# Performance work log

Measured on AMD Instinct MI355X. Metric: run time of the kernel, lower is better.

Reference implementation:

```python
import jax, jax.numpy as jnp
import numpy as np

NUM_HEADS = 8

def setup_inputs() -> dict:
    key = jax.random.key(0)
    ks = jax.random.split(key, 8)
    B, T, J, N, C = 4, 16, 17, 17, 256
    x = jax.random.normal(ks[0], (B, T, J, N, C), dtype=jnp.float32)
    A_s = jax.random.uniform(ks[1], (J, J), dtype=jnp.float32)
    A_v = jax.random.uniform(ks[2], (N, N), dtype=jnp.float32)
    W_qkv = jax.random.normal(ks[3], (C, 5 * C), dtype=jnp.float32) * (C ** -0.5)
    W_proj = jax.random.normal(ks[4], (3 * C, C), dtype=jnp.float32) * ((3 * C) ** -0.5)
    b_proj = jnp.zeros((C,), dtype=jnp.float32)
    # M ~ xavier_uniform(gain=1.414) over shape (1, J, N, C)
    bound = 1.414 * np.sqrt(6.0 / (N + C))
    M = jax.random.uniform(ks[5], (1, J, N, C), dtype=jnp.float32, minval=-bound, maxval=bound)
    adj_s = jnp.full((J, J), 1e-6, dtype=jnp.float32)  # torch stores (1,1,J,J); broadcast-identical
    adj_v = jnp.full((N, N), 1e-6, dtype=jnp.float32)
    return {"x": x, "A_s": A_s, "A_v": A_v, "W_qkv": W_qkv, "W_proj": W_proj,
            "b_proj": b_proj, "M": M, "adj_s": adj_s, "adj_v": adj_v}


def reference(x, A_s, A_v, W_qkv, W_proj, b_proj, M, adj_s, adj_v):
    B, T, J, N, C = x.shape
    h = NUM_HEADS
    hc = C // h
    scale = hc ** -0.5
    bt = B * T
    xr = x.reshape(bt, J, N, C)
    # qkv Linear (no bias) then view(..., C, 5): channel-interleaved split
    qkv = (xr @ W_qkv).reshape(bt, J, N, C, 5)
    q, k, vs, vv, vsv = (qkv[..., i] * M for i in range(5))
    def heads(t):
        return t.reshape(bt, J, N, h, hc)
    q, k, vs, vv, vsv = map(heads, (q, k, vs, vv, vsv))
    # spatial attention over joints j (per node n), temporal/variate attention over n (per j)
    att_s_o = jnp.einsum('bjnhc,bknhc->bhnjk', q, k) * scale   # (bt,h,N,J,J)
    att_v_o = jnp.einsum('bjnhc,bjmhc->bhjnm', q, k) * scale   # (bt,h,J,N,N)
    att_s = jax.nn.softmax(att_s_o, axis=-1)
    att_v = jax.nn.softmax(att_v_o, axis=-1)
    # outer-product combine, algebraically separated:
    # x_vsv[b,j,n,:] = sum_{k,m} att_s[b,h,n,j,k] * att_v[b,h,j,n,m] * vsv[b,k,m,h,:]
    r = jnp.einsum('bhjnm,bkmhc->bhjnkc', att_v, vsv)           # (bt,h,J,N,J,hc)
    x_vsv = jnp.einsum('bhnjk,bhjnkc->bjnhc', att_s, r).reshape(bt, J, N, C)
    # adjacency-biased attentions (symmetrized learned bias + fixed adjacency)
    adjs = A_s + adj_s
    adjs = (adjs.T + adjs) * 0.5
    adjv = A_v + adj_v
    adjv = (adjv.T + adjv) * 0.5
    att_s2 = jax.nn.softmax(att_s_o + adjs, axis=-1)
    att_v2 = jax.nn.softmax(att_v_o + adjv, axis=-1)
    x_vs = jnp.einsum('bhnjk,bknhc->bjnhc', att_s2, vs).reshape(bt, J, N, C)
    x_vv = jnp.einsum('bhjnm,bjmhc->bjnhc', att_v2, vv).reshape(bt, J, N, C)
    out = jnp.concatenate([x_vsv, x_vs, x_vv], axis=-1) @ W_proj + b_proj
    return out.reshape(B, T, J, N, C)
```

## Files before the change

### kernel.cpp

```cpp
#include <hip/hip_runtime.h>
#include <math.h>

#define ROWS 18496
#define SCALE 0.17677669529663687f

typedef unsigned short ushort_t;
typedef __attribute__((ext_vector_type(8))) short short8;
typedef __attribute__((ext_vector_type(4))) float f32x4;

__device__ __forceinline__ void fma4(float4& d, float s, const float4& v) {
    d.x = fmaf(s, v.x, d.x); d.y = fmaf(s, v.y, d.y);
    d.z = fmaf(s, v.z, d.z); d.w = fmaf(s, v.w, d.w);
}
__device__ __forceinline__ float dot4(const float4& a, const float4& b) {
    return a.x*b.x + a.y*b.y + a.z*b.z + a.w*b.w;
}

__device__ __forceinline__ ushort_t f2bf(float x) {
    union { float f; unsigned u; } v; v.f = x;
    unsigned r = v.u + 0x7fffu + ((v.u >> 16) & 1u);
    return (ushort_t)(r >> 16);
}
__device__ __forceinline__ float bf2f(ushort_t b) {
    union { unsigned u; float f; } v; v.u = ((unsigned)b) << 16; return v.f;
}

__device__ __forceinline__ unsigned cvtpk(float a, float b) {
    unsigned r;
    asm("v_cvt_pk_bf16_f32 %0, %1, %2" : "=v"(r) : "v"(a), "v"(b));
    return r;
}
__device__ __forceinline__ float uasf(unsigned u) {
    union { unsigned u; float f; } v; v.u = u; return v.f;
}

__device__ __forceinline__ void gl_lds16(const void* g, void* l) {
    __builtin_amdgcn_global_load_lds(
        (const __attribute__((address_space(1))) void*)g,
        (__attribute__((address_space(3))) void*)l, 16, 0, 0);
}

__device__ __forceinline__ void store_hilo(ushort_t* yhi, ushort_t* ylo,
                                           size_t off, const float4& a)
{
    unsigned h01 = cvtpk(a.x, a.y), h23 = cvtpk(a.z, a.w);
    unsigned l01 = cvtpk(a.x - uasf(h01 << 16), a.y - uasf(h01 & 0xffff0000u));
    unsigned l23 = cvtpk(a.z - uasf(h23 << 16), a.w - uasf(h23 & 0xffff0000u));
    *(uint2*)&yhi[off] = (uint2){h01, h23};
    *(uint2*)&ylo[off] = (uint2){l01, l23};
}

__global__ __launch_bounds__(256) void k_cvt_w(
    const float* __restrict__ W, ushort_t* __restrict__ bh, ushort_t* __restrict__ bl,
    const float* __restrict__ Wp, ushort_t* __restrict__ wph, ushort_t* __restrict__ wpl)
{
    if (blockIdx.x < 1280) {
        int o = blockIdx.x;
        int kk = threadIdx.x;
        int col = (o & 255) * 5 + (o >> 8);
        float v = W[(size_t)kk * 1280 + col];
        ushort_t hh = f2bf(v);
        bh[(size_t)o * 256 + kk] = hh;
        bl[(size_t)o * 256 + kk] = f2bf(v - bf2f(hh));
    } else {
        int n = blockIdx.x - 1280;
        for (int k = threadIdx.x; k < 768; k += 256) {
            float v = Wp[(size_t)k * 256 + n];
            ushort_t h = f2bf(v);
            wph[(size_t)n * 768 + k] = h;
            wpl[(size_t)n * 768 + k] = f2bf(v - bf2f(h));
        }
    }
}

template<int BM, int BN, int K, int MODE>
__global__ __launch_bounds__(256) void k_gemm(
    const float* __restrict__ Af,
    const ushort_t* __restrict__ Ahi, const ushort_t* __restrict__ Alo,
    const ushort_t* __restrict__ Bhi, const ushort_t* __restrict__ Blo,
    const float* __restrict__ aux,
    float* __restrict__ out)
{
    constexpr int MT = BM / 32;
    constexpr int NT = BN / 32;
    __shared__ __attribute__((aligned(16))) ushort_t sAh[BM * 32];
    __shared__ __attribute__((aligned(16))) ushort_t sAl[BM * 32];
    __shared__ __attribute__((aligned(16))) ushort_t sBh[BN * 32];
    __shared__ __attribute__((aligned(16))) ushort_t sBl[BN * 32];

    const int t = threadIdx.x;
    const int lane = t & 63;
    const int ln = lane & 15, quad = lane >> 4;
    const int wave = t >> 6;
    const int wm = wave >> 1, wn = wave & 1;

    const int nwg = (int)(gridDim.x * gridDim.y);
    int wgid = (int)(blockIdx.y * gridDim.x + blockIdx.x);
    int q = nwg >> 3, r = nwg & 7;
    int xcd = wgid & 7, i0 = wgid >> 3;
    int base = (xcd < r) ? xcd * (q + 1) : r * (q + 1) + (xcd - r) * q;
    int logical = base + i0;
    const int m0 = (logical / (int)gridDim.x) * BM;
    const int n0 = (logical % (int)gridDim.x) * BN;

    f32x4 acc[MT][NT];
#pragma unroll
    for (int i = 0; i < MT; ++i)
#pragma unroll
        for (int j = 0; j < NT; ++j) acc[i][j] = (f32x4){0.f, 0.f, 0.f, 0.f};

    float4 a0r, a1r, a2r, a3r;
    size_t a_base = 0;
    if (MODE == 0) {
        int row = t >> 1, kc8 = t & 1;
        int gr = m0 + row; if (gr > ROWS - 1) gr = ROWS - 1;
        a_base = (size_t)gr * K + kc8 * 16;
        const float* src = &Af[a_base];
        a0r = *(const float4*)&src[0];
        a1r = *(const float4*)&src[4];
        a2r = *(const float4*)&src[8];
        a3r = *(const float4*)&src[12];
    }

    for (int kb = 0; kb < K; kb += 32) {
        __syncthreads();
        if (MODE == 0) {
            unsigned h0 = cvtpk(a0r.x, a0r.y), h1 = cvtpk(a0r.z, a0r.w);
            unsigned h2 = cvtpk(a1r.x, a1r.y), h3 = cvtpk(a1r.z, a1r.w);
            unsigned h4 = cvtpk(a2r.x, a2r.y), h5 = cvtpk(a2r.z, a2r.w);
            unsigned h6 = cvtpk(a3r.x, a3r.y), h7 = cvtpk(a3r.z, a3r.w);
            unsigned l0 = cvtpk(a0r.x - uasf(h0 << 16), a0r.y - uasf(h0 & 0xffff0000u));
            unsigned l1 = cvtpk(a0r.z - uasf(h1 << 16), a0r.w - uasf(h1 & 0xffff0000u));
            unsigned l2 = cvtpk(a1r.x - uasf(h2 << 16), a1r.y - uasf(h2 & 0xffff0000u));
            unsigned l3 = cvtpk(a1r.z - uasf(h3 << 16), a1r.w - uasf(h3 & 0xffff0000u));
            unsigned l4 = cvtpk(a2r.x - uasf(h4 << 16), a2r.y - uasf(h4 & 0xffff0000u));
            unsigned l5 = cvtpk(a2r.z - uasf(h5 << 16), a2r.w - uasf(h5 & 0xffff0000u));
            unsigned l6 = cvtpk(a3r.x - uasf(h6 << 16), a3r.y - uasf(h6 & 0xffff0000u));
            unsigned l7 = cvtpk(a3r.z - uasf(h7 << 16), a3r.w - uasf(h7 & 0xffff0000u));
            uint4* dh = (uint4*)((char*)sAh + (size_t)t * 32);
            uint4* dl = (uint4*)((char*)sAl + (size_t)t * 32);
            dh[0] = (uint4){h0, h1, h2, h3};
            dh[1] = (uint4){h4, h5, h6, h7};
            dl[0] = (uint4){l0, l1, l2, l3};
            dl[1] = (uint4){l4, l5, l6, l7};
        } else {
#pragma unroll
            for (int s = t; s < BM * 4; s += 256) {
                int row = s >> 2, kc = s & 3;
                int gr = m0 + row; if (gr > ROWS - 1) gr = ROWS - 1;
                size_t gb = ((size_t)gr * K + kb) * 2 + kc * 16;
                int lb = (s & ~63) * 16;
                gl_lds16((const char*)Ahi + gb, (char*)sAh + lb);
                gl_lds16((const char*)Alo + gb, (char*)sAl + lb);
            }
        }
#pragma unroll
        for (int s = t; s < BN * 4; s += 256) {
            int row = s >> 2, kc = s & 3;
            size_t gb = ((size_t)(n0 + row) * K + kb) * 2 + kc * 16;
            int lb = (s & ~63) * 16;
            gl_lds16((const char*)Bhi + gb, (char*)sBh + lb);
            gl_lds16((const char*)Blo + gb, (char*)sBl + lb);
        }
        __syncthreads();

        if (MODE == 0 && kb + 32 < K) {
            const float* src = &Af[a_base + kb + 32];
            a0r = *(const float4*)&src[0];
            a1r = *(const float4*)&src[4];
            a2r = *(const float4*)&src[8];
            a3r = *(const float4*)&src[12];
        }

        short8 ah[MT], al[MT], bh[NT], bl[NT];
#pragma unroll
        for (int i = 0; i < MT; ++i) {
            int off = (wm * (BM / 2) + i * 16 + ln) * 32 + quad * 8;
            ah[i] = *(const short8*)&sAh[off];
            al[i] = *(const short8*)&sAl[off];
        }
#pragma unroll
        for (int j = 0; j < NT; ++j) {
            int off = (wn * (BN / 2) + j * 16 + ln) * 32 + quad * 8;
            bh[j] = *(const short8*)&sBh[off];
            bl[j] = *(const short8*)&sBl[off];
        }
#pragma unroll
        for (int i = 0; i < MT; ++i)
#pragma unroll
            for (int j = 0; j < NT; ++j) {
                acc[i][j] = __builtin_amdgcn_mfma_f32_16x16x32_bf16(ah[i], bh[j], acc[i][j], 0, 0, 0);
                acc[i][j] = __builtin_amdgcn_mfma_f32_16x16x32_bf16(ah[i], bl[j], acc[i][j], 0, 0, 0);
                acc[i][j] = __builtin_amdgcn_mfma_f32_16x16x32_bf16(al[i], bh[j], acc[i][j], 0, 0, 0);
            }
    }

#pragma unroll
    for (int i = 0; i < MT; ++i) {
#pragma unroll
        for (int r2 = 0; r2 < 4; ++r2) {
            int gm = m0 + wm * (BM / 2) + i * 16 + quad * 4 + r2;
            if (gm >= ROWS) continue;
            if (MODE == 0) {
                int jn = gm % 289;
                const float* Mrow = &aux[(size_t)jn * 256];
#pragma unroll
                for (int j = 0; j < NT; ++j) {
                    int gn = n0 + wn * (BN / 2) + j * 16 + ln;
                    out[(size_t)gm * 1280 + gn] = acc[i][j][r2] * Mrow[gn & 255];
                }
            } else {
#pragma unroll
                for (int j = 0; j < NT; ++j) {
                    int gn = n0 + wn * (BN / 2) + j * 16 + ln;
                    out[(size_t)gm * 256 + gn] = acc[i][j][r2] + aux[gn];
                }
            }
        }
    }
}

__global__ __launch_bounds__(512, 4) void k_att(
    const float* __restrict__ qkv5,
    const float* __restrict__ A_s, const float* __restrict__ A_v,
    const float* __restrict__ adjS, const float* __restrict__ adjV,
    ushort_t* __restrict__ yhi, ushort_t* __restrict__ ylo)
{
    __shared__ __attribute__((aligned(16))) float sm[17340];
    float* aS  = sm;
    float* aV  = sm + 4913;
    float* ebS = sm + 9826;
    float* ebV = sm + 10115;
    float* buf = sm + 10404;

    const int t  = threadIdx.x;
    const int bh = blockIdx.x;
    const int b  = bh >> 3, h = bh & 7;
    const size_t rowbase = (size_t)b * 289;

    for (int idx = t; idx < 578; idx += 512) {
        int f = idx / 289, rem = idx % 289;
        int jj = rem / 17, kk = rem % 17;
        float bias;
        if (f == 0)
            bias = 0.5f * ((A_s[jj*17+kk] + adjS[jj*17+kk]) + (A_s[kk*17+jj] + adjS[kk*17+jj]));
        else
            bias = 0.5f * ((A_v[jj*17+kk] + adjV[jj*17+kk]) + (A_v[kk*17+jj] + adjV[kk*17+jj]));
        (f ? ebV : ebS)[rem] = expf(bias);
    }

    for (int ch = 0; ch < 2; ++ch) {
        __syncthreads();
        for (int idx = t; idx < 1156; idx += 512) {
            int p = idx >> 2, c = idx & 3;
            *(float4*)&buf[p * 20 + c * 4] =
                *(const float4*)&qkv5[(rowbase + p) * 1280 + 256 + h * 32 + ch * 16 + c * 4];
        }
        __syncthreads();
        for (int u = t; u < 578; u += 512) {
            const bool isS = (u < 289);
            const int p = isS ? u : u - 289;
            const float* qp = &qkv5[(rowbase + p) * 1280 + h * 32 + ch * 16];
            float4 q0 = *(const float4*)&qp[0];
            float4 q1 = *(const float4*)&qp[4];
            float4 q2 = *(const float4*)&qp[8];
            float4 q3 = *(const float4*)&qp[12];
            const int a = p / 17, bb = p % 17;
            if (isS) {
                float* dst = &aS[bb * 289 + a * 17];
#pragma unroll
                for (int kk = 0; kk < 17; ++kk) {
                    const float4* r = (const float4*)&buf[(kk * 17 + bb) * 20];
                    float val = dot4(q0, r[0]) + dot4(q1, r[1]) + dot4(q2, r[2]) + dot4(q3, r[3]);
                    if (ch == 0) dst[kk] = val; else dst[kk] += val;
                }
            } else {
                float* dst = &aV[a * 289 + bb * 17];
#pragma unroll
                for (int mm = 0; mm < 17; ++mm) {
                    const float4* r = (const float4*)&buf[(a * 17 + mm) * 20];
                    float val = dot4(q0, r[0]) + dot4(q1, r[1]) + dot4(q2, r[2]) + dot4(q3, r[3]);
                    if (ch == 0) dst[mm] = val; else dst[mm] += val;
                }
            }
        }
    }
    __syncthreads();

    for (int idx = t; idx < 578; idx += 512) {
        float* row = (idx < 289) ? &aS[idx * 17] : &aV[(idx - 289) * 17];
        float mx = row[0];
#pragma unroll
        for (int kk = 1; kk < 17; ++kk) mx = fmaxf(mx, row[kk]);
        float sum = 0.f;
#pragma unroll
        for (int kk = 0; kk < 17; ++kk) {
            float e = expf((row[kk] - mx) * SCALE);
            row[kk] = e; sum += e;
        }
        float inv = 1.f / sum;
#pragma unroll
        for (int kk = 0; kk < 17; ++kk) row[kk] *= inv;
    }

    {
        const int lane = t & 63;
        const int ln = lane & 15, quad = lane >> 4;
        const int wave = t >> 6;
        ushort_t* vh = (ushort_t*)buf;
        ushort_t* vl = vh + 32 * 168;

        f32x4 acc[3][2];
#pragma unroll
        for (int r = 0; r < 3; ++r) {
            acc[r][0] = (f32x4){0.f,0.f,0.f,0.f};
            acc[r][1] = (f32x4){0.f,0.f,0.f,0.f};
        }

        int sbase[3], vbase[3];
#pragma unroll
        for (int r = 0; r < 3; ++r) {
            int p = (wave + 8 * r) * 16 + ln; if (p > 288) p = 288;
            int jj = (p * 61681) >> 20;
            int nn = p - jj * 17;
            sbase[r] = nn * 289 + jj * 17;
            vbase[r] = jj * 289 + nn * 17;
        }

        for (int khalf = 0; khalf < 2; ++khalf) {
            const int qbase = khalf * 160;
            const int V = khalf ? 129 : 160;
            __syncthreads();
            if (khalf == 1) {
                uint4* z = (uint4*)vh;
                for (int e = t; e < 1344; e += 512) z[e] = (uint4){0,0,0,0};
                __syncthreads();
            }
            for (int e = t; e < 32 * V; e += 512) {
                int ql = e >> 5, c = e & 31;
                float v = qkv5[(rowbase + qbase + ql) * 1280 + 1024 + h * 32 + c];
                unsigned hp = cvtpk(v, v);
                float lo = v - uasf(hp << 16);
                unsigned lp = cvtpk(lo, lo);
                vh[c * 168 + ql] = (ushort_t)hp;
                vl[c * 168 + ql] = (ushort_t)lp;
            }
            __syncthreads();
#pragma unroll
            for (int kstep = 0; kstep < 5; ++kstep) {
                const int q0 = qbase + kstep * 32 + quad * 8;
                const int lb = kstep * 32 + quad * 8;
#pragma unroll
                for (int r = 0; r < 3; ++r) {
                    if (r == 2 && wave >= 3) continue;
                    union { short8 s; unsigned u[4]; } A, L;
                    int qc0 = (q0 < 289) ? q0 : 288;
                    int k17 = (qc0 * 61681) >> 20;
                    int m17 = qc0 - k17 * 17;
                    float sv = aS[sbase[r] + k17];
#pragma unroll
                    for (int i2 = 0; i2 < 4; ++i2) {
                        float pv0 = sv * aV[vbase[r] + m17];
                        ++m17; if (m17 == 17) { m17 = 0; ++k17; sv = aS[sbase[r] + k17]; }
                        float pv1 = sv * aV[vbase[r] + m17];
                        ++m17; if (m17 == 17) { m17 = 0; ++k17; sv = aS[sbase[r] + k17]; }
                        if (khalf == 1) {
                            if (q0 + 2 * i2     >= 289) pv0 = 0.f;
                            if (q0 + 2 * i2 + 1 >= 289) pv1 = 0.f;
                        }
                        unsigned hp = cvtpk(pv0, pv1);
                        unsigned lp = cvtpk(pv0 - uasf(hp << 16),
                                            pv1 - uasf(hp & 0xffff0000u));
                        A.u[i2] = hp; L.u[i2] = lp;
                    }
#pragma unroll
                    for (int ct = 0; ct < 2; ++ct) {
                        short8 bh8 = *(const short8*)&vh[(ct * 16 + ln) * 168 + lb];
                        short8 bl8 = *(const short8*)&vl[(ct * 16 + ln) * 168 + lb];
                        acc[r][ct] = __builtin_amdgcn_mfma_f32_16x16x32_bf16(A.s, bh8, acc[r][ct], 0, 0, 0);
                        acc[r][ct] = __builtin_amdgcn_mfma_f32_16x16x32_bf16(A.s, bl8, acc[r][ct], 0, 0, 0);
                        acc[r][ct] = __builtin_amdgcn_mfma_f32_16x16x32_bf16(L.s, bh8, acc[r][ct], 0, 0, 0);
                    }
                }
            }
        }
#pragma unroll
        for (int r = 0; r < 3; ++r) {
            int rt = wave + 8 * r;
            if (rt >= 19) continue;
#pragma unroll
            for (int ct = 0; ct < 2; ++ct) {
#pragma unroll
                for (int rr = 0; rr < 4; ++rr) {
                    int p = rt * 16 + quad * 4 + rr;
                    if (p > 288) continue;
                    float v = acc[r][ct][rr];
                    unsigned hp = cvtpk(v, v);
                    float lo = v - uasf(hp << 16);
                    unsigned lp = cvtpk(lo, lo);
                    size_t off = (rowbase + p) * 768 + h * 32 + ct * 16 + ln;
                    yhi[off] = (ushort_t)hp;
                    ylo[off] = (ushort_t)lp;
                }
            }
        }
    }

    __syncthreads();
    for (int idx = t; idx < 578; idx += 512) {
        float* row;
        const float* eb;
        if (idx < 289) { row = &aS[idx * 17]; eb = &ebS[(idx % 17) * 17]; }
        else { int i2 = idx - 289; row = &aV[i2 * 17]; eb = &ebV[(i2 % 17) * 17]; }
        float s = 0.f;
#pragma unroll
        for (int kk = 0; kk < 17; ++kk) { float wv = row[kk] * eb[kk]; row[kk] = wv; s += wv; }
        float inv = 1.f / s;
#pragma unroll
        for (int kk = 0; kk < 17; ++kk) row[kk] *= inv;
    }

    for (int ch = 0; ch < 2; ++ch) {
        __syncthreads();
        for (int idx = t; idx < 1156; idx += 512) {
            int p = idx >> 2, c = idx & 3;
            *(float4*)&buf[p * 24 + c * 4] =
                *(const float4*)&qkv5[(rowbase + p) * 1280 + 512 + h * 32 + ch * 16 + c * 4];
        }
        __syncthreads();
        for (int u = t; u < 1156; u += 512) {
            const int c4 = (u & 3) * 4, rest = u >> 2;
            const int n = rest % 17, j = rest / 17;
            const float* as = &aS[n * 289 + j * 17];
            float4 a0 = {0,0,0,0};
            for (int kk = 0; kk < 17; ++kk) {
                float4 v = *(const float4*)&buf[(kk * 17 + n) * 24 + c4];
                fma4(a0, as[kk], v);
            }
            store_hilo(yhi, ylo, (rowbase + j * 17 + n) * 768 + 256 + h * 32 + ch * 16 + c4, a0);
        }
    }

    for (int ch = 0; ch < 2; ++ch) {
        __syncthreads();
        for (int idx = t; idx < 1156; idx += 512) {
            int p = idx >> 2, c = idx & 3;
            *(float4*)&buf[p * 24 + c * 4] =
                *(const float4*)&qkv5[(rowbase + p) * 1280 + 768 + h * 32 + ch * 16 + c * 4];
        }
        __syncthreads();
        for (int u = t; u < 1156; u += 512) {
            const int c4 = (u & 3) * 4, rest = u >> 2;
            const int j = rest % 17, n = rest / 17;
            const float* av = &aV[j * 289 + n * 17];
            float4 a0 = {0,0,0,0};
            for (int mm = 0; mm < 17; ++mm) {
                float4 v = *(const float4*)&buf[(j * 17 + mm) * 24 + c4];
                fma4(a0, av[mm], v);
            }
            store_hilo(yhi, ylo, (rowbase + j * 17 + n) * 768 + 512 + h * 32 + ch * 16 + c4, a0);
        }
    }
}

extern "C" void kernel_launch(void* const* d_in, const int* in_sizes, int n_in,
                              void* d_out, int out_size, void* d_ws, size_t ws_size,
                              hipStream_t stream)
{
    const float* x    = (const float*)d_in[0];
    const float* A_s  = (const float*)d_in[1];
    const float* A_v  = (const float*)d_in[2];
    const float* Wqkv = (const float*)d_in[3];
    const float* Wp   = (const float*)d_in[4];
    const float* bp   = (const float*)d_in[5];
    const float* M    = (const float*)d_in[6];
    const float* adjS = (const float*)d_in[7];
    const float* adjV = (const float*)d_in[8];
    float* out = (float*)d_out;

    char* w = (char*)d_ws;
    float*    qkv5  = (float*)w;
    ushort_t* wph   = (ushort_t*)(w + 94699520);
    ushort_t* wpl   = (ushort_t*)(w + 94699520 + 393216);
    char* R = w + 134946816;
    ushort_t* wqh = (ushort_t*)(R + 18939904);
    ushort_t* wql = (ushort_t*)(R + 19595264);
    ushort_t* yhi = (ushort_t*)R;
    ushort_t* ylo = (ushort_t*)(R + 28422144);

    k_cvt_w<<<dim3(1536), 256, 0, stream>>>(Wqkv, wqh, wql, Wp, wph, wpl);
    k_gemm<128, 128, 256, 0><<<dim3(10, 145), 256, 0, stream>>>(x, nullptr, nullptr,
                                                                wqh, wql, M, qkv5);
    k_att<<<dim3(512), 512, 0, stream>>>(qkv5, A_s, A_v, adjS, adjV, yhi, ylo);
    k_gemm<128, 64, 768, 1><<<dim3(4, 145), 256, 0, stream>>>(nullptr, yhi, ylo,
                                                              wph, wpl, bp, out);
}
```

Baseline: 249.8 us.

## Compute attention logits with split-bf16 MFMA plus scalar edge fixup

Replaces the LDS-staged FP32 dot-product loop for the spatial and variate attention scores with 16x16x32 bf16 MFMA tiles per wave. Q and K are split into high and low bf16 parts and combined over three MFMAs to approximate FP32 accuracy. The 17th row and column of each 17x17 block, which do not fit in the 16x16 tile, are computed separately with scalar FP32 dot products. This removes two LDS staging passes and their barriers, at the cost of extra conversion work and a slight precision change.

```diff
diff --git a/kernel.cpp b/kernel.cpp
--- a/kernel.cpp
+++ b/kernel.cpp
@@ -249,40 +249,66 @@
         (f ? ebV : ebS)[rem] = expf(bias);
     }
 
-    for (int ch = 0; ch < 2; ++ch) {
-        __syncthreads();
-        for (int idx = t; idx < 1156; idx += 512) {
-            int p = idx >> 2, c = idx & 3;
-            *(float4*)&buf[p * 20 + c * 4] =
-                *(const float4*)&qkv5[(rowbase + p) * 1280 + 256 + h * 32 + ch * 16 + c * 4];
-        }
-        __syncthreads();
-        for (int u = t; u < 578; u += 512) {
-            const bool isS = (u < 289);
-            const int p = isS ? u : u - 289;
-            const float* qp = &qkv5[(rowbase + p) * 1280 + h * 32 + ch * 16];
-            float4 q0 = *(const float4*)&qp[0];
-            float4 q1 = *(const float4*)&qp[4];
-            float4 q2 = *(const float4*)&qp[8];
-            float4 q3 = *(const float4*)&qp[12];
-            const int a = p / 17, bb = p % 17;
-            if (isS) {
-                float* dst = &aS[bb * 289 + a * 17];
-#pragma unroll
-                for (int kk = 0; kk < 17; ++kk) {
-                    const float4* r = (const float4*)&buf[(kk * 17 + bb) * 20];
-                    float val = dot4(q0, r[0]) + dot4(q1, r[1]) + dot4(q2, r[2]) + dot4(q3, r[3]);
-                    if (ch == 0) dst[kk] = val; else dst[kk] += val;
-                }
-            } else {
-                float* dst = &aV[a * 289 + bb * 17];
-#pragma unroll
-                for (int mm = 0; mm < 17; ++mm) {
-                    const float4* r = (const float4*)&buf[(a * 17 + mm) * 20];
-                    float val = dot4(q0, r[0]) + dot4(q1, r[1]) + dot4(q2, r[2]) + dot4(q3, r[3]);
-                    if (ch == 0) dst[mm] = val; else dst[mm] += val;
-                }
-            }
+    {
+        const int lane = t & 63;
+        const int ln = lane & 15, quad = lane >> 4;
+        const int wave = t >> 6;
+        const float* qb = &qkv5[rowbase * 1280 + h * 32];
+        const float* kb = &qkv5[rowbase * 1280 + 256 + h * 32];
+
+        for (int g = wave; g < 34; g += 8) {
+            const bool isV = (g < 17);
+            const int gg = isV ? g : g - 17;
+            const int rp = isV ? (gg * 17 + ln) : (ln * 17 + gg);
+            const float* qsrc = &qb[(size_t)rp * 1280 + quad * 8];
+            const float* ksrc = &kb[(size_t)rp * 1280 + quad * 8];
+            float4 qv0 = *(const float4*)&qsrc[0];
+            float4 qv1 = *(const float4*)&qsrc[4];
+            float4 kv0 = *(const float4*)&ksrc[0];
+            float4 kv1 = *(const float4*)&ksrc[4];
+            union { short8 s; unsigned u[4]; } Ah, Al, Bh, Bl;
+            Ah.u[0] = cvtpk(qv0.x, qv0.y); Ah.u[1] = cvtpk(qv0.z, qv0.w);
+            Ah.u[2] = cvtpk(qv1.x, qv1.y); Ah.u[3] = cvtpk(qv1.z, qv1.w);
+            Al.u[0] = cvtpk(qv0.x - uasf(Ah.u[0] << 16), qv0.y - uasf(Ah.u[0] & 0xffff0000u));
+            Al.u[1] = cvtpk(qv0.z - uasf(Ah.u[1] << 16), qv0.w - uasf(Ah.u[1] & 0xffff0000u));
+            Al.u[2] = cvtpk(qv1.x - uasf(Ah.u[2] << 16), qv1.y - uasf(Ah.u[2] & 0xffff0000u));
+            Al.u[3] = cvtpk(qv1.z - uasf(Ah.u[3] << 16), qv1.w - uasf(Ah.u[3] & 0xffff0000u));
+            Bh.u[0] = cvtpk(kv0.x, kv0.y); Bh.u[1] = cvtpk(kv0.z, kv0.w);
+            Bh.u[2] = cvtpk(kv1.x, kv1.y); Bh.u[3] = cvtpk(kv1.z, kv1.w);
+            Bl.u[0] = cvtpk(kv0.x - uasf(Bh.u[0] << 16), kv0.y - uasf(Bh.u[0] & 0xffff0000u));
+            Bl.u[1] = cvtpk(kv0.z - uasf(Bh.u[1] << 16), kv0.w - uasf(Bh.u[1] & 0xffff0000u));
+            Bl.u[2] = cvtpk(kv1.x - uasf(Bh.u[2] << 16), kv1.y - uasf(Bh.u[2] & 0xffff0000u));
+            Bl.u[3] = cvtpk(kv1.z - uasf(Bh.u[3] << 16), kv1.w - uasf(Bh.u[3] & 0xffff0000u));
+            f32x4 acc = (f32x4){0.f, 0.f, 0.f, 0.f};
+            acc = __builtin_amdgcn_mfma_f32_16x16x32_bf16(Ah.s, Bh.s, acc, 0, 0, 0);
+            acc = __builtin_amdgcn_mfma_f32_16x16x32_bf16(Ah.s, Bl.s, acc, 0, 0, 0);
+            acc = __builtin_amdgcn_mfma_f32_16x16x32_bf16(Al.s, Bh.s, acc, 0, 0, 0);
+            float* dst = (isV ? aV : aS) + gg * 289;
+#pragma unroll
+            for (int i = 0; i < 4; ++i) {
+                int row = quad * 4 + i;
+                dst[row * 17 + ln] = acc[i];
+            }
+        }
+
+        for (int e = t; e < 1122; e += 512) {
+            int g = e / 33, s = e % 33;
+            const bool isV = (g < 17);
+            const int gg = isV ? g : g - 17;
+            int rr = (s < 17) ? 16 : (s - 17);
+            int cc = (s < 17) ? s : 16;
+            int qp2 = isV ? (gg * 17 + rr) : (rr * 17 + gg);
+            int kp2 = isV ? (gg * 17 + cc) : (cc * 17 + gg);
+            const float* qsrc = &qb[(size_t)qp2 * 1280];
+            const float* ksrc = &kb[(size_t)kp2 * 1280];
+            float acc = 0.f;
+#pragma unroll
+            for (int c8 = 0; c8 < 8; ++c8) {
+                float4 qv = *(const float4*)&qsrc[c8 * 4];
+                float4 kv = *(const float4*)&ksrc[c8 * 4];
+                acc += dot4(qv, kv);
+            }
+            (isV ? aV : aS)[gg * 289 + rr * 17 + cc] = acc;
         }
     }
     __syncthreads();
```

New measurement: 251.7 us. Within noise of the previous version (+0.7%).
